# Kernel optimization log

Measured on AMD Instinct MI355X. Metric: run time of the kernel, lower is better.

## Reference

```python
import jax, jax.numpy as jnp
import numpy as np

VOCAB, EMB, MAXPOS, HID, IMG, ATT = 30522, 768, 512, 512, 2048, 256
LN_EPS = 1e-12


def bert_embed(ids, word_emb, pos_emb, type_emb, ln_g, ln_b):
    # ids: [..., L]; BERT embeddings = word + position + token_type(0), then LayerNorm
    L = ids.shape[-1]
    x = word_emb[ids] + pos_emb[:L] + type_emb[0]
    mu = jnp.mean(x, axis=-1, keepdims=True)
    var = jnp.mean((x - mu) ** 2, axis=-1, keepdims=True)
    return ln_g * (x - mu) * jax.lax.rsqrt(var + LN_EPS) + ln_b


def setup_inputs() -> dict:
    key = jax.random.key(0)
    ks = jax.random.split(key, 24)
    B, L, S, H = 32, 512, 6, 128
    u = lambda k, shape: jax.random.uniform(k, shape, jnp.float32, -0.1, 0.1)
    inp = {
        "separate_images": jax.random.normal(ks[0], (B, S, IMG), jnp.float32),
        "img_pred": jax.random.normal(ks[1], (B, IMG), jnp.float32),
        "input_text": jax.random.randint(ks[2], (B, L), 0, VOCAB),
        "prev_hist": jax.random.randint(ks[3], (B, S, H), 0, VOCAB),
        "prev_hist_len": jax.random.randint(ks[4], (B, S), 0, H),
        "masks": jnp.zeros((B, L), dtype=bool),
        # BERT embedding params
        "word_emb": jax.random.normal(ks[5], (VOCAB, EMB), jnp.float32) * 0.02,
        "pos_emb": jax.random.normal(ks[6], (MAXPOS, EMB), jnp.float32) * 0.02,
        "type_emb": jax.random.normal(ks[7], (2, EMB), jnp.float32) * 0.02,
        "ln_g": jnp.ones((EMB,), jnp.float32),
        "ln_b": jnp.zeros((EMB,), jnp.float32),
        # model linears (weights stored input-major: [in, out])
        "W_sep": u(ks[8], (IMG, HID)), "b_sep": jnp.zeros((HID,), jnp.float32),
        "W_e2h": u(ks[9], (EMB, HID)), "b_e2h": jnp.zeros((HID,), jnp.float32),
        "W_hist": u(ks[10], (EMB, HID)), "b_hist": jnp.zeros((HID,), jnp.float32),
        "W_img": u(ks[11], (IMG, HID)), "b_img": jnp.zeros((HID,), jnp.float32),
        "W_mm": u(ks[12], (2 * HID, HID)), "b_mm": jnp.zeros((HID,), jnp.float32),
        "W_a1": u(ks[13], (HID, ATT)), "b_a1": jnp.zeros((ATT,), jnp.float32),
        "W_a2": u(ks[14], (ATT, 1)), "b_a2": jnp.zeros((1,), jnp.float32),
        "W_f1": u(ks[15], (2 * HID, HID)), "b_f1": jnp.zeros((HID,), jnp.float32),
        "W_f2": u(ks[16], (HID, 2)), "b_f2": jnp.zeros((2,), jnp.float32),
    }
    return inp


def reference(separate_images, img_pred, input_text, prev_hist, prev_hist_len, masks,
              word_emb, pos_emb, type_emb, ln_g, ln_b,
              W_sep, b_sep, W_e2h, b_e2h, W_hist, b_hist, W_img, b_img,
              W_mm, b_mm, W_a1, b_a1, W_a2, b_a2, W_f1, b_f1, W_f2, b_f2):
    relu = jax.nn.relu
    # utterance path
    reps = bert_embed(input_text, word_emb, pos_emb, type_emb, ln_g, ln_b)  # [B,L,E]
    input_reps = relu(reps @ W_e2h + b_e2h)                                 # [B,L,H]
    proj_img = relu(img_pred @ W_img + b_img)                               # [B,H]
    rep_img = jnp.broadcast_to(proj_img[:, None, :], input_reps.shape)
    mm_reps = relu(jnp.concatenate([input_reps, rep_img], axis=2) @ W_mm + b_mm)
    att = jnp.tanh(mm_reps @ W_a1 + b_a1) @ W_a2 + b_a2                     # [B,L,1]
    att = jnp.where(masks[:, :, None], -jnp.inf, att)
    w = jax.nn.softmax(att, axis=1)
    attended = jnp.sum(mm_reps * w, axis=1)                                 # [B,H]
    # image / history path
    sep = separate_images @ W_sep + b_sep                                   # [B,6,H]
    H = prev_hist.shape[-1]
    hist_emb = bert_embed(prev_hist, word_emb, pos_emb, type_emb, ln_g, ln_b)  # [B,6,Hl,E]
    valid = (jnp.arange(H) < prev_hist_len[..., None]).astype(hist_emb.dtype)  # [B,6,Hl]
    denom = jnp.maximum(prev_hist_len, 1).astype(hist_emb.dtype)[..., None]
    hist_avg = jnp.einsum('bshe,bsh->bse', hist_emb, valid) / denom
    contrib = relu(hist_avg @ W_hist + b_hist) * (prev_hist_len[..., None] > 0)
    sep = relu(sep + contrib)
    sep = sep / jnp.maximum(jnp.linalg.norm(sep, axis=2, keepdims=True), 1e-12)
    sep = sep.mean(axis=1)                                                  # [B,H]
    h = jnp.concatenate([sep, attended], axis=1) @ W_f1 + b_f1
    h = jax.nn.gelu(h, approximate=False)
    return h @ W_f2 + b_f2
```

## Files before the change

kernel.cpp:

```cpp
#include <hip/hip_runtime.h>
#include <hip/hip_bf16.h>
#include <math.h>

#define VOCAB 30522
#define EMB 768
#define MAXPOS 512
#define HID 512
#define IMG 2048
#define ATT 256
#define BB 32
#define LL 512
#define SS 6
#define HL 128
#define LN_EPS 1e-12f
#define KCH 128
#define NROWS (BB * LL)
#define MPS (BB + BB * SS)

typedef __bf16 bf16_t;
typedef __attribute__((ext_vector_type(4))) __bf16 bf16x4;
typedef __attribute__((ext_vector_type(8))) __bf16 bf16x8;
typedef __attribute__((ext_vector_type(4))) float f32x4;

#define AS1 __attribute__((address_space(1)))
#define AS3 __attribute__((address_space(3)))
__device__ __forceinline__ void gload_lds16(const bf16_t* g, bf16_t* l) {
    __builtin_amdgcn_global_load_lds((const AS1 void*)g, (AS3 void*)l, 16, 0, 0);
}

__device__ __forceinline__ float wave_sum(float v) {
    v += __shfl_xor(v, 1);  v += __shfl_xor(v, 2);  v += __shfl_xor(v, 4);
    v += __shfl_xor(v, 8);  v += __shfl_xor(v, 16); v += __shfl_xor(v, 32);
    return v;
}
__device__ __forceinline__ float wave_max(float v) {
    v = fmaxf(v, __shfl_xor(v, 1));  v = fmaxf(v, __shfl_xor(v, 2));
    v = fmaxf(v, __shfl_xor(v, 4));  v = fmaxf(v, __shfl_xor(v, 8));
    v = fmaxf(v, __shfl_xor(v, 16)); v = fmaxf(v, __shfl_xor(v, 32));
    return v;
}


__device__ void dev_embed2(int r0, const int* __restrict__ ids,
                           const float* __restrict__ we, const float* __restrict__ pe,
                           const float* __restrict__ te, const float* __restrict__ g,
                           const float* __restrict__ bta, bf16_t* __restrict__ out) {
    int lane = threadIdx.x & 63;
    int r1 = r0 + 1;
    int id0 = ids[r0], id1 = ids[r1];
    const float* w0 = we + (size_t)id0 * EMB + lane * 12;
    const float* p0 = pe + (size_t)(r0 & (LL - 1)) * EMB + lane * 12;
    const float* w1 = we + (size_t)id1 * EMB + lane * 12;
    const float* p1 = pe + (size_t)(r1 & (LL - 1)) * EMB + lane * 12;
    const float* tp = te + lane * 12;
    float4 a0[3], b0[3], a1[3], b1[3], c[3];
#pragma unroll
    for (int q = 0; q < 3; q++) {
        a0[q] = *(const float4*)(w0 + q * 4);
        a1[q] = *(const float4*)(w1 + q * 4);
        b0[q] = *(const float4*)(p0 + q * 4);
        b1[q] = *(const float4*)(p1 + q * 4);
        c[q]  = *(const float4*)(tp + q * 4);
    }
    const float* gp = g + lane * 12;
    const float* bp = bta + lane * 12;
#pragma unroll
    for (int rr = 0; rr < 2; rr++) {
        float4* av = rr ? a1 : a0;
        float4* bv = rr ? b1 : b0;
        int r = rr ? r1 : r0;
        float x[12]; float s = 0.f, ss = 0.f;
#pragma unroll
        for (int q = 0; q < 3; q++) {
            float v0 = av[q].x + bv[q].x + c[q].x;
            float v1 = av[q].y + bv[q].y + c[q].y;
            float v2 = av[q].z + bv[q].z + c[q].z;
            float v3 = av[q].w + bv[q].w + c[q].w;
            x[q * 4 + 0] = v0; x[q * 4 + 1] = v1;
            x[q * 4 + 2] = v2; x[q * 4 + 3] = v3;
            s += v0 + v1 + v2 + v3;
            ss += v0 * v0 + v1 * v1 + v2 * v2 + v3 * v3;
        }
        s = wave_sum(s); ss = wave_sum(ss);
        float mu = s * (1.0f / EMB);
        float var = ss * (1.0f / EMB) - mu * mu;
        float rs = rsqrtf(var + LN_EPS);
        bf16_t* orow = out + (size_t)r * EMB + lane * 12;
#pragma unroll
        for (int q = 0; q < 3; q++) {
            float4 gv = *(const float4*)(gp + q * 4);
            float4 bb = *(const float4*)(bp + q * 4);
            bf16x4 y;
            y[0] = (bf16_t)(gv.x * (x[q * 4 + 0] - mu) * rs + bb.x);
            y[1] = (bf16_t)(gv.y * (x[q * 4 + 1] - mu) * rs + bb.y);
            y[2] = (bf16_t)(gv.z * (x[q * 4 + 2] - mu) * rs + bb.z);
            y[3] = (bf16_t)(gv.w * (x[q * 4 + 3] - mu) * rs + bb.w);
            *(bf16x4*)(orow + q * 4) = y;
        }
    }
}

__device__ void dev_conv(const float* __restrict__ in, bf16_t* __restrict__ out,
                         int K, int N, int x, int y, char* smem) {
    float (*t)[33] = (float(*)[33])smem;
    int n0 = x * 32, k0 = y * 32;
    int tx = threadIdx.x & 31, ty = threadIdx.x >> 5;
#pragma unroll
    for (int i = 0; i < 4; i++)
        t[ty + i * 8][tx] = in[(size_t)(k0 + ty + i * 8) * N + n0 + tx];
    __syncthreads();
#pragma unroll
    for (int i = 0; i < 4; i++)
        out[(size_t)(n0 + ty + i * 8) * K + k0 + tx] = (bf16_t)t[tx][ty + i * 8];
}

__device__ void dev_hist(int bs, int grp, const int* __restrict__ ids,
                         const int* __restrict__ lens,
                         const float* __restrict__ we, const float* __restrict__ pe,
                         const float* __restrict__ te, const float* __restrict__ g,
                         const float* __restrict__ bta,
                         float* __restrict__ parts, char* smem) {
    float (*acc)[EMB] = (float(*)[EMB])smem;
    int len = lens[bs];
    int tid = threadIdx.x, wid = tid >> 6, lane = tid & 63;
#pragma unroll
    for (int k = 0; k < 12; k++) acc[wid][lane + k * 64] = 0.f;
#pragma unroll
    for (int i = 0; i < 4; i++) {
        int h = grp + 8 * wid + 32 * i;
        if (h >= len) continue;
        int id = ids[bs * HL + h];
        const float* wrow = we + (size_t)id * EMB;
        const float* prow = pe + (size_t)h * EMB;
        float x[12]; float s = 0.f, ss = 0.f;
#pragma unroll
        for (int k = 0; k < 12; k++) {
            int j = lane + k * 64;
            float v = wrow[j] + prow[j] + te[j];
            x[k] = v; s += v; ss += v * v;
        }
        s = wave_sum(s); ss = wave_sum(ss);
        float mu = s * (1.0f / EMB);
        float var = ss * (1.0f / EMB) - mu * mu;
        float rs = rsqrtf(var + LN_EPS);
#pragma unroll
        for (int k = 0; k < 12; k++) {
            int j = lane + k * 64;
            acc[wid][j] += g[j] * (x[k] - mu) * rs + bta[j];
        }
    }
    __syncthreads();
    float* dst = parts + ((size_t)grp * (BB * SS) + bs) * EMB;
    for (int j = tid; j < EMB; j += 256)
        dst[j] = acc[0][j] + acc[1][j] + acc[2][j] + acc[3][j];
}

template <int AMODE>
__device__ void dev_thin(int bx, int by, int bz,
                         const float* __restrict__ A, int lda,
                         const float* __restrict__ parts, size_t MNp,
                         const float* __restrict__ abias,
                         const int* __restrict__ lens,
                         const float* __restrict__ B, int ldb,
                         float* __restrict__ part, int M, int N, char* smem) {
    float (*As)[KCH] = (float(*)[KCH])smem;
    int tid = threadIdx.x;
    int n0 = bx * 256, m0 = by * 16, k0 = bz * KCH;

    if (AMODE == 0) {
#pragma unroll
        for (int i = 0; i < 2; i++) {
            int lin = (i * 256 + tid) * 4;
            int m = lin >> 7, k = lin & (KCH - 1);
            *(float4*)&As[m][k] = *(const float4*)(A + (size_t)(m0 + m) * lda + k0 + k);
        }
    } else if (AMODE == 1) {
#pragma unroll
        for (int i = 0; i < 2; i++) {
            int f = i * 256 + tid;
            int m = f >> 5, kq = (f & 31) * 4;
            int row = m0 + m;
            float4 v = *(const float4*)(abias + k0 + kq);
#pragma unroll
            for (int ks = 0; ks < 16; ks++) {
                float4 p = *(const float4*)(parts + (size_t)ks * MNp +
                                            (size_t)row * 512 + k0 + kq);
                v.x += p.x; v.y += p.y; v.z += p.z; v.w += p.w;
            }
            v.x = fmaxf(v.x, 0.f); v.y = fmaxf(v.y, 0.f);
            v.z = fmaxf(v.z, 0.f); v.w = fmaxf(v.w, 0.f);
            *(float4*)&As[m][kq] = v;
        }
    } else {
#pragma unroll
        for (int i = 0; i < 2; i++) {
            int f = i * 256 + tid;
            int m = f >> 5, kq = (f & 31) * 4;
            int row = m0 + m;
            float invd = 1.0f / fmaxf((float)lens[row], 1.0f);
            float4 v = {};
#pragma unroll
            for (int gg = 0; gg < 8; gg++) {
                float4 p = *(const float4*)(parts + (size_t)gg * MNp +
                                            (size_t)row * EMB + k0 + kq);
                v.x += p.x; v.y += p.y; v.z += p.z; v.w += p.w;
            }
            As[m][kq + 0] = v.x * invd; As[m][kq + 1] = v.y * invd;
            As[m][kq + 2] = v.z * invd; As[m][kq + 3] = v.w * invd;
        }
    }
    __syncthreads();
    int nq = tid & 63, mg = tid >> 6;
    const float* Bp = B + (size_t)k0 * ldb + n0 + nq * 4;
    float4 acc[4] = {};
    for (int kk = 0; kk < KCH; kk += 8) {
        float4 b0 = *(const float4*)(Bp + (size_t)(kk + 0) * ldb);
        float4 b1 = *(const float4*)(Bp + (size_t)(kk + 1) * ldb);
        float4 b2 = *(const float4*)(Bp + (size_t)(kk + 2) * ldb);
        float4 b3 = *(const float4*)(Bp + (size_t)(kk + 3) * ldb);
        float4 b4 = *(const float4*)(Bp + (size_t)(kk + 4) * ldb);
        float4 b5 = *(const float4*)(Bp + (size_t)(kk + 5) * ldb);
        float4 b6 = *(const float4*)(Bp + (size_t)(kk + 6) * ldb);
        float4 b7 = *(const float4*)(Bp + (size_t)(kk + 7) * ldb);
        float4 bv[8] = {b0, b1, b2, b3, b4, b5, b6, b7};
#pragma unroll
        for (int j = 0; j < 8; j++) {
#pragma unroll
            for (int mi = 0; mi < 4; mi++) {
                float a = As[mg * 4 + mi][kk + j];
                acc[mi].x += a * bv[j].x; acc[mi].y += a * bv[j].y;
                acc[mi].z += a * bv[j].z; acc[mi].w += a * bv[j].w;
            }
        }
    }
    size_t MN = (size_t)M * N;
#pragma unroll
    for (int mi = 0; mi < 4; mi++)
        *(float4*)(part + (size_t)bz * MN +
                   (size_t)(m0 + mg * 4 + mi) * N + n0 + nq * 4) = acc[mi];
}

template <int ACT, bool OBF16, bool ROWADD4, bool FUSE_ATT>
__device__ void dev_mfma(int bx, int by,
                         const bf16_t* __restrict__ A, const bf16_t* __restrict__ Bt,
                         const float* __restrict__ bias,
                         const float* __restrict__ rowadd,
                         void* __restrict__ Cv,
                         const float* __restrict__ w2, float* __restrict__ att_part,
                         int M, int N, int K, char* smem) {
    bf16_t* As = (bf16_t*)smem;
    bf16_t* Bs = (bf16_t*)(smem + 16384);
    float (*attp)[2] = (float(*)[2])(smem + 32768);
    int tid = threadIdx.x;
    int lane = tid & 63, wid = tid >> 6;
    int wr = wid >> 1, wc = wid & 1;
    int row0 = by * 128, col0 = bx * 128;

    int srow = tid >> 2;
    int sslot = tid & 3;

    const bf16_t* Ag = A + (size_t)row0 * K;
    const bf16_t* Bg = Bt + (size_t)col0 * K;

    f32x4 acc[4][4] = {};
    int lrow = lane & 15;
    int g8 = lane >> 4;

    auto stage_pair = [&](int buf, int kb) {
#pragma unroll
        for (int rr = 0; rr < 2; rr++) {
            int r = srow + rr * 64;
            int sl = sslot ^ ((r >> 1) & 3);
            gload_lds16(Ag + (size_t)r * K + kb + sl * 8,
                        As + buf * 4096 + wid * 512 + rr * 2048);
            gload_lds16(Bg + (size_t)r * K + kb + sl * 8,
                        Bs + buf * 4096 + wid * 512 + rr * 2048);
        }
    };

    stage_pair(0, 0);
    __syncthreads();
    int cur = 0;
    for (int kb = 0; kb < K; kb += 32) {
        if (kb + 32 < K) stage_pair(cur ^ 1, kb + 32);
        bf16x8 af[4], bfr[4];
#pragma unroll
        for (int mi = 0; mi < 4; mi++) {
            int r = wr * 64 + mi * 16 + lrow;
            int sl = g8 ^ ((r >> 1) & 3);
            af[mi] = *(const bf16x8*)(As + cur * 4096 + r * 32 + sl * 8);
        }
#pragma unroll
        for (int ni = 0; ni < 4; ni++) {
            int r = wc * 64 + ni * 16 + lrow;
            int sl = g8 ^ ((r >> 1) & 3);
            bfr[ni] = *(const bf16x8*)(Bs + cur * 4096 + r * 32 + sl * 8);
        }
#pragma unroll
        for (int mi = 0; mi < 4; mi++)
#pragma unroll
            for (int ni = 0; ni < 4; ni++)
                acc[mi][ni] = __builtin_amdgcn_mfma_f32_16x16x32_bf16(
                    af[mi], bfr[ni], acc[mi][ni], 0, 0, 0);
        __syncthreads();
        cur ^= 1;
    }

    if (FUSE_ATT) {
        float w2v[4];
#pragma unroll
        for (int ni = 0; ni < 4; ni++)
            w2v[ni] = w2[col0 + wc * 64 + ni * 16 + lrow];
#pragma unroll
        for (int mi = 0; mi < 4; mi++) {
#pragma unroll
            for (int r = 0; r < 4; r++) {
                float s = 0.f;
#pragma unroll
                for (int ni = 0; ni < 4; ni++) {
                    int col = col0 + wc * 64 + ni * 16 + lrow;
                    float v = tanhf(acc[mi][ni][r] + bias[col]);
                    s += v * w2v[ni];
                }
                s += __shfl_xor(s, 1); s += __shfl_xor(s, 2);
                s += __shfl_xor(s, 4); s += __shfl_xor(s, 8);
                if ((lane & 15) == 0)
                    attp[wr * 64 + mi * 16 + (lane >> 4) * 4 + r][wc] = s;
            }
        }
        __syncthreads();
        if (tid < 128)
            att_part[(size_t)bx * M + row0 + tid] = attp[tid][0] + attp[tid][1];
        return;
    }

    float* Cf = (float*)Cv;
    bf16_t* Cb = (bf16_t*)Cv;
    int rg = (lane >> 4) * 4;
#pragma unroll
    for (int mi = 0; mi < 4; mi++) {
#pragma unroll
        for (int ni = 0; ni < 4; ni++) {
            int col = col0 + wc * 64 + ni * 16 + lrow;
#pragma unroll
            for (int r = 0; r < 4; r++) {
                int row = row0 + wr * 64 + mi * 16 + rg + r;
                float v = acc[mi][ni][r] + bias[col];
                if (ROWADD4) {
                    int bslot = row >> 9;
#pragma unroll
                    for (int ks = 0; ks < 4; ks++)
                        v += rowadd[(size_t)ks * BB * HID + (size_t)bslot * HID + col];
                }
                if (ACT == 1) v = fmaxf(v, 0.f);
                if (ACT == 2) v = tanhf(v);
                if (OBF16) Cb[(size_t)row * N + col] = (bf16_t)v;
                else       Cf[(size_t)row * N + col] = v;
            }
        }
    }
}


#define D1_EMB   2048
#define D1_HIST  (D1_EMB + 1536)
#define D1_CONV  (D1_HIST + 768)
#define D1_T4A   (D1_CONV + 64)
#define D1_T4B   (D1_T4A + 384)
__global__ __launch_bounds__(256)
void uber_pre(const int* input_text, const int* prev_hist, const int* prev_hist_ln,
              const float* word_emb, const float* pos_emb, const float* type_emb,
              const float* ln_g, const float* ln_b,
              const float* W_e2h, bf16_t* Wt_e2h,
              const float* W_mm, bf16_t* Wt_mm,
              const float* W_a1, bf16_t* Wt_a1,
              const float* img_pred, const float* sep_images,
              const float* W_img, const float* W_sep,
              bf16_t* reps_bf, float* hist_parts, float* partA) {
    __shared__ __align__(16) char smem[12288];
    int bid = blockIdx.x;
    if (bid < D1_EMB) {
        int r0 = (bid * 4 + (threadIdx.x >> 6)) * 2;
        dev_embed2(r0, input_text, word_emb, pos_emb, type_emb, ln_g, ln_b, reps_bf);
    } else if (bid < D1_HIST) {
        int b = bid - D1_EMB;
        dev_hist(b >> 3, b & 7, prev_hist, prev_hist_ln, word_emb, pos_emb,
                 type_emb, ln_g, ln_b, hist_parts, smem);
    } else if (bid < D1_CONV) {
        int b = bid - D1_HIST;
        if (b < 384)      dev_conv(W_e2h, Wt_e2h, EMB, HID, b & 15, b >> 4, smem);
        else if (b < 640) { int c = b - 384; dev_conv(W_mm, Wt_mm, HID, HID, c & 15, c >> 4, smem); }
        else              { int c = b - 640; dev_conv(W_a1, Wt_a1, HID, ATT, c & 7, c >> 3, smem); }
    } else if (bid < D1_T4A) {
        int l = bid - D1_CONV;
        dev_thin<0>(l & 1, (l >> 1) & 1, l >> 2, img_pred, IMG,
                    nullptr, 0, nullptr, nullptr, W_img, HID, partA, MPS, HID, smem);
    } else {
        int l = bid - D1_T4A;
        int l2 = l >> 1;
        dev_thin<0>(l & 1, l2 % 12, l2 / 12, sep_images, IMG,
                    nullptr, 0, nullptr, nullptr, W_sep, HID,
                    partA + (size_t)BB * HID, MPS, HID, smem);
    }
}

#define D2_MF   512
#define D2_IMG2 (D2_MF + 16)
#define D2_HG   (D2_IMG2 + 144)
__global__ __launch_bounds__(256)
void uber_gemm1(const bf16_t* reps_bf, const bf16_t* Wt_e2h, const float* b_e2h,
                bf16_t* input_reps,
                const float* partA, const float* b_img, const float* W_mm,
                float* partC,
                const float* hist_parts, const int* prev_hist_ln,
                const float* W_hist, float* partB) {
    __shared__ __align__(16) char smem[33792];
    int bid = blockIdx.x;
    if (bid < D2_MF) {
        dev_mfma<1, true, false, false>(bid & 3, bid >> 2, reps_bf, Wt_e2h, b_e2h,
                                        nullptr, input_reps, nullptr, nullptr,
                                        NROWS, HID, EMB, smem);
    } else if (bid < D2_IMG2) {
        int l = bid - D2_MF;
        dev_thin<1>(l & 1, (l >> 1) & 1, l >> 2, nullptr, 0,
                    partA, (size_t)MPS * HID, b_img, nullptr,
                    W_mm + (size_t)HID * HID, HID, partC, BB, HID, smem);
    } else {
        int l = bid - D2_IMG2;
        int l2 = l >> 1;
        dev_thin<2>(l & 1, l2 % 12, l2 / 12, nullptr, 0,
                    hist_parts, (size_t)BB * SS * EMB, nullptr, prev_hist_ln,
                    W_hist, HID, partB, BB * SS, HID, smem);
    }
}

__global__ __launch_bounds__(256)
void mfma_mm_k(const bf16_t* input_reps, const bf16_t* Wt_mm, const float* b_mm,
               const float* partC, bf16_t* mm_reps) {
    __shared__ __align__(16) char smem[33792];
    dev_mfma<1, true, true, false>(blockIdx.x & 3, blockIdx.x >> 2, input_reps,
                                   Wt_mm, b_mm, partC, mm_reps, nullptr, nullptr,
                                   NROWS, HID, HID, smem);
}

__global__ __launch_bounds__(256)
void mfma_a1_k(const bf16_t* mm_reps, const bf16_t* Wt_a1, const float* b_a1,
               const float* W_a2, float* att_part) {
    __shared__ __align__(16) char smem[33792];
    dev_mfma<2, false, false, true>(blockIdx.x & 1, blockIdx.x >> 1, mm_reps,
                                    Wt_a1, b_a1, nullptr, nullptr, W_a2, att_part,
                                    NROWS, ATT, HID, smem);
}

__global__ void attend_sep(const float* __restrict__ att_part,
                           const unsigned char* __restrict__ masks,
                           const float* __restrict__ b2,
                           const bf16_t* __restrict__ mm,
                           const float* __restrict__ pA,
                           const float* __restrict__ pB,
                           const float* __restrict__ b_sep,
                           const float* __restrict__ b_hist,
                           const int* __restrict__ lens,
                           float* __restrict__ xcat) {
    int bid = blockIdx.x;
    int tid = threadIdx.x, wid = tid >> 6, lane = tid & 63;
    __shared__ float wsm[LL];
    __shared__ float arr[4];
    __shared__ float red[4][64];
    if (bid < 256) {
        int b = bid >> 3, hc = bid & 7;
        int l0 = tid, l1 = tid + 256;
        float v0 = att_part[b * LL + l0] + att_part[(size_t)NROWS + b * LL + l0] + b2[0];
        float v1 = att_part[b * LL + l1] + att_part[(size_t)NROWS + b * LL + l1] + b2[0];
        if (masks[b * LL + l0]) v0 = -INFINITY;
        if (masks[b * LL + l1]) v1 = -INFINITY;
        float m = wave_max(fmaxf(v0, v1));
        if (lane == 0) arr[wid] = m;
        __syncthreads();
        float M = fmaxf(fmaxf(arr[0], arr[1]), fmaxf(arr[2], arr[3]));
        float e0 = expf(v0 - M), e1 = expf(v1 - M);
        wsm[l0] = e0; wsm[l1] = e1;
        float s = wave_sum(e0 + e1);
        __syncthreads();
        if (lane == 0) arr[wid] = s;
        __syncthreads();
        float inv = 1.0f / (arr[0] + arr[1] + arr[2] + arr[3]);
        int h = hc * 64 + lane;
        const bf16_t* base = mm + (size_t)b * LL * HID + h;
        float acc = 0.f;
        int ls = wid * 128;
#pragma unroll 4
        for (int l = ls; l < ls + 128; l++)
            acc += (float)base[(size_t)l * HID] * wsm[l];
        red[wid][lane] = acc;
        __syncthreads();
        if (wid == 0)
            xcat[b * 1024 + 512 + h] =
                (red[0][lane] + red[1][lane] + red[2][lane] + red[3][lane]) * inv;
    } else {
        int b = bid - 256;
        const size_t MNa = (size_t)MPS * HID;
        const size_t MNb = (size_t)BB * SS * HID;
        float acc0 = 0.f, acc1 = 0.f;
        for (int s = 0; s < SS; s++) {
            int idx = b * SS + s;
            int len = lens[idx];
            size_t baseA = (size_t)(BB + idx) * HID;
            size_t baseB = (size_t)idx * HID;
            float v0 = b_sep[tid], v1 = b_sep[tid + 256];
#pragma unroll
            for (int ks = 0; ks < 16; ks++) {
                v0 += pA[ks * MNa + baseA + tid];
                v1 += pA[ks * MNa + baseA + tid + 256];
            }
            float c0 = b_hist[tid], c1 = b_hist[tid + 256];
#pragma unroll
            for (int ks = 0; ks < 6; ks++) {
                c0 += pB[ks * MNb + baseB + tid];
                c1 += pB[ks * MNb + baseB + tid + 256];
            }
            c0 = fmaxf(c0, 0.f); c1 = fmaxf(c1, 0.f);
            if (len <= 0) { c0 = 0.f; c1 = 0.f; }
            float y0 = fmaxf(v0 + c0, 0.f), y1 = fmaxf(v1 + c1, 0.f);
            float ssq = wave_sum(y0 * y0 + y1 * y1);
            if (lane == 0) arr[wid] = ssq;
            __syncthreads();
            float tot = arr[0] + arr[1] + arr[2] + arr[3];
            float inv = 1.0f / fmaxf(sqrtf(tot), 1e-12f);
            acc0 += y0 * inv; acc1 += y1 * inv;
            __syncthreads();
        }
        xcat[b * 1024 + tid] = acc0 * (1.0f / SS);
        xcat[b * 1024 + 256 + tid] = acc1 * (1.0f / SS);
    }
}

__global__ __launch_bounds__(256)
void thin_f1_k(const float* xcat, const float* W_f1, float* partD) {
    __shared__ __align__(16) char smem[8192];
    int l = blockIdx.x;
    dev_thin<0>(l & 1, (l >> 1) & 1, l >> 2, xcat, 1024,
                nullptr, 0, nullptr, nullptr, W_f1, HID, partD, BB, HID, smem);
}

__global__ void final_out2(const float* __restrict__ part,
                           const float* __restrict__ b1,
                           const float* __restrict__ W2,
                           const float* __restrict__ b2,
                           float* __restrict__ out) {
    int b = blockIdx.x;
    int tid = threadIdx.x;
    __shared__ float h[HID];
    const size_t MN = (size_t)BB * HID;
#pragma unroll
    for (int jj = 0; jj < 2; jj++) {
        int d = tid + jj * 256;
        float a = b1[d];
#pragma unroll
        for (int ks = 0; ks < 8; ks++) a += part[ks * MN + (size_t)b * HID + d];
        h[d] = 0.5f * a * (1.0f + erff(a * 0.70710678118654752f));
    }
    __syncthreads();
    float p0 = 0.f, p1 = 0.f;
    for (int j = tid; j < HID; j += 256) {
        float hv = h[j];
        p0 += hv * W2[j * 2 + 0];
        p1 += hv * W2[j * 2 + 1];
    }
    p0 = wave_sum(p0); p1 = wave_sum(p1);
    __shared__ float r0[4], r1[4];
    int wid = tid >> 6;
    if ((tid & 63) == 0) { r0[wid] = p0; r1[wid] = p1; }
    __syncthreads();
    if (tid == 0) {
        out[b * 2 + 0] = r0[0] + r0[1] + r0[2] + r0[3] + b2[0];
        out[b * 2 + 1] = r1[0] + r1[1] + r1[2] + r1[3] + b2[1];
    }
}

extern "C" void kernel_launch(void* const* d_in, const int* in_sizes, int n_in,
                              void* d_out, int out_size, void* d_ws, size_t ws_size,
                              hipStream_t stream) {
    const float* sep_images   = (const float*)d_in[0];
    const float* img_pred     = (const float*)d_in[1];
    const int*   input_text   = (const int*)d_in[2];
    const int*   prev_hist    = (const int*)d_in[3];
    const int*   prev_hist_ln = (const int*)d_in[4];
    const unsigned char* masks = (const unsigned char*)d_in[5];
    const float* word_emb = (const float*)d_in[6];
    const float* pos_emb  = (const float*)d_in[7];
    const float* type_emb = (const float*)d_in[8];
    const float* ln_g = (const float*)d_in[9];
    const float* ln_b = (const float*)d_in[10];
    const float* W_sep = (const float*)d_in[11]; const float* b_sep = (const float*)d_in[12];
    const float* W_e2h = (const float*)d_in[13]; const float* b_e2h = (const float*)d_in[14];
    const float* W_hist = (const float*)d_in[15]; const float* b_hist = (const float*)d_in[16];
    const float* W_img = (const float*)d_in[17]; const float* b_img = (const float*)d_in[18];
    const float* W_mm = (const float*)d_in[19]; const float* b_mm = (const float*)d_in[20];
    const float* W_a1 = (const float*)d_in[21]; const float* b_a1 = (const float*)d_in[22];
    const float* W_a2 = (const float*)d_in[23]; const float* b_a2 = (const float*)d_in[24];
    const float* W_f1 = (const float*)d_in[25]; const float* b_f1 = (const float*)d_in[26];
    const float* W_f2 = (const float*)d_in[27]; const float* b_f2 = (const float*)d_in[28];

    char* ws = (char*)d_ws;
    size_t o = 0;
    auto alloc = [&](size_t bytes) { void* p = ws + o; o += (bytes + 255) & ~(size_t)255; return p; };

    bf16_t* reps_bf     = (bf16_t*)alloc((size_t)NROWS * EMB * 2);
    bf16_t* input_reps  = (bf16_t*)alloc((size_t)NROWS * HID * 2);
    bf16_t* mm_reps     = (bf16_t*)alloc((size_t)NROWS * HID * 2);
    float*  att_part    = (float*)alloc((size_t)2 * NROWS * 4);
    float*  xcat        = (float*)alloc((size_t)BB * 1024 * 4);
    float*  hist_parts  = (float*)alloc((size_t)8 * BB * SS * EMB * 4);
    bf16_t* Wt_e2h      = (bf16_t*)alloc((size_t)EMB * HID * 2);
    bf16_t* Wt_mm       = (bf16_t*)alloc((size_t)HID * HID * 2);
    bf16_t* Wt_a1       = (bf16_t*)alloc((size_t)HID * ATT * 2);
    float*  partA       = (float*)alloc((size_t)16 * MPS * HID * 4);
    float*  partB       = (float*)alloc((size_t)6 * BB * SS * HID * 4);
    float*  partC       = (float*)alloc((size_t)4 * BB * HID * 4);
    float*  partD       = (float*)alloc((size_t)8 * BB * HID * 4);

    uber_pre<<<D1_T4B, 256, 0, stream>>>(
        input_text, prev_hist, prev_hist_ln, word_emb, pos_emb, type_emb,
        ln_g, ln_b, W_e2h, Wt_e2h, W_mm, Wt_mm, W_a1, Wt_a1,
        img_pred, sep_images, W_img, W_sep, reps_bf, hist_parts, partA);

    uber_gemm1<<<D2_HG, 256, 0, stream>>>(
        reps_bf, Wt_e2h, b_e2h, input_reps,
        partA, b_img, W_mm, partC,
        hist_parts, prev_hist_ln, W_hist, partB);

    mfma_mm_k<<<512, 256, 0, stream>>>(input_reps, Wt_mm, b_mm, partC, mm_reps);

    mfma_a1_k<<<256, 256, 0, stream>>>(mm_reps, Wt_a1, b_a1, W_a2, att_part);

    attend_sep<<<288, 256, 0, stream>>>(att_part, masks, b_a2, mm_reps,
                                        partA, partB, b_sep, b_hist,
                                        prev_hist_ln, xcat);

    thin_f1_k<<<32, 256, 0, stream>>>(xcat, W_f1, partD);

    final_out2<<<BB, 256, 0, stream>>>(partD, b_f1, W_f2, b_f2, (float*)d_out);
}
```

Baseline: 144.5 us.

## Rebalance fused kernel stages to overlap history work with GEMMs

Moves the history-embedding LayerNorm and the separate-image thin GEMM out of the first fused kernel into the e2h GEMM kernel. Moves the history-projection thin GEMM into the mm GEMM kernel, which drops one separate launch. The aim is to balance per-stage work so memory-bound blocks run beside compute-bound MFMA blocks, and to lower the first kernel's shared memory. This adds more heterogeneous blocks to each launch, which can cause tail imbalance or contention for LDS and occupancy.

```diff
diff --git a/kernel.cpp b/kernel.cpp
--- a/kernel.cpp
+++ b/kernel.cpp
@@ -362,85 +362,92 @@
 }
 
 
-#define D1_EMB   2048
-#define D1_HIST  (D1_EMB + 1536)
-#define D1_CONV  (D1_HIST + 768)
-#define D1_T4A   (D1_CONV + 64)
-#define D1_T4B   (D1_T4A + 384)
+#define E1_EMB   2048
+#define E1_CONV  (E1_EMB + 768)
+#define E1_TIMG  (E1_CONV + 64)
 __global__ __launch_bounds__(256)
-void uber_pre(const int* input_text, const int* prev_hist, const int* prev_hist_ln,
+void uber_pre(const int* input_text,
               const float* word_emb, const float* pos_emb, const float* type_emb,
               const float* ln_g, const float* ln_b,
               const float* W_e2h, bf16_t* Wt_e2h,
               const float* W_mm, bf16_t* Wt_mm,
               const float* W_a1, bf16_t* Wt_a1,
-              const float* img_pred, const float* sep_images,
-              const float* W_img, const float* W_sep,
-              bf16_t* reps_bf, float* hist_parts, float* partA) {
-    __shared__ __align__(16) char smem[12288];
+              const float* img_pred, const float* W_img,
+              bf16_t* reps_bf, float* partA) {
+    __shared__ __align__(16) char smem[8192];
     int bid = blockIdx.x;
-    if (bid < D1_EMB) {
+    if (bid < E1_EMB) {
         int r0 = (bid * 4 + (threadIdx.x >> 6)) * 2;
         dev_embed2(r0, input_text, word_emb, pos_emb, type_emb, ln_g, ln_b, reps_bf);
-    } else if (bid < D1_HIST) {
-        int b = bid - D1_EMB;
-        dev_hist(b >> 3, b & 7, prev_hist, prev_hist_ln, word_emb, pos_emb,
-                 type_emb, ln_g, ln_b, hist_parts, smem);
-    } else if (bid < D1_CONV) {
-        int b = bid - D1_HIST;
+    } else if (bid < E1_CONV) {
+        int b = bid - E1_EMB;
         if (b < 384)      dev_conv(W_e2h, Wt_e2h, EMB, HID, b & 15, b >> 4, smem);
         else if (b < 640) { int c = b - 384; dev_conv(W_mm, Wt_mm, HID, HID, c & 15, c >> 4, smem); }
         else              { int c = b - 640; dev_conv(W_a1, Wt_a1, HID, ATT, c & 7, c >> 3, smem); }
-    } else if (bid < D1_T4A) {
-        int l = bid - D1_CONV;
+    } else {
+        int l = bid - E1_CONV;
         dev_thin<0>(l & 1, (l >> 1) & 1, l >> 2, img_pred, IMG,
                     nullptr, 0, nullptr, nullptr, W_img, HID, partA, MPS, HID, smem);
-    } else {
-        int l = bid - D1_T4A;
+    }
+}
+
+#define E2_MF   512
+#define E2_HIST (E2_MF + 1536)
+#define E2_SEP  (E2_HIST + 384)
+#define E2_IMG2 (E2_SEP + 16)
+__global__ __launch_bounds__(256)
+void uber_gemm1(const bf16_t* reps_bf, const bf16_t* Wt_e2h, const float* b_e2h,
+                bf16_t* input_reps,
+                const int* prev_hist, const int* prev_hist_ln,
+                const float* word_emb, const float* pos_emb, const float* type_emb,
+                const float* ln_g, const float* ln_b, float* hist_parts,
+                const float* sep_images, const float* W_sep,
+                float* partA, const float* b_img, const float* W_mm,
+                float* partC) {
+    __shared__ __align__(16) char smem[33792];
+    int bid = blockIdx.x;
+    if (bid < E2_MF) {
+        dev_mfma<1, true, false, false>(bid & 3, bid >> 2, reps_bf, Wt_e2h, b_e2h,
+                                        nullptr, input_reps, nullptr, nullptr,
+                                        NROWS, HID, EMB, smem);
+    } else if (bid < E2_HIST) {
+        int b = bid - E2_MF;
+        dev_hist(b >> 3, b & 7, prev_hist, prev_hist_ln, word_emb, pos_emb,
+                 type_emb, ln_g, ln_b, hist_parts, smem);
+    } else if (bid < E2_SEP) {
+        int l = bid - E2_HIST;
         int l2 = l >> 1;
         dev_thin<0>(l & 1, l2 % 12, l2 / 12, sep_images, IMG,
                     nullptr, 0, nullptr, nullptr, W_sep, HID,
                     partA + (size_t)BB * HID, MPS, HID, smem);
-    }
-}
-
-#define D2_MF   512
-#define D2_IMG2 (D2_MF + 16)
-#define D2_HG   (D2_IMG2 + 144)
+    } else {
+        int l = bid - E2_SEP;
+        dev_thin<1>(l & 1, (l >> 1) & 1, l >> 2, nullptr, 0,
+                    partA, (size_t)MPS * HID, b_img, nullptr,
+                    W_mm + (size_t)HID * HID, HID, partC, BB, HID, smem);
+    }
+}
+
+#define E3_MF 512
+#define E3_HG (E3_MF + 144)
 __global__ __launch_bounds__(256)
-void uber_gemm1(const bf16_t* reps_bf, const bf16_t* Wt_e2h, const float* b_e2h,
-                bf16_t* input_reps,
-                const float* partA, const float* b_img, const float* W_mm,
-                float* partC,
+void uber_gemm2(const bf16_t* input_reps, const bf16_t* Wt_mm, const float* b_mm,
+                const float* partC, bf16_t* mm_reps,
                 const float* hist_parts, const int* prev_hist_ln,
                 const float* W_hist, float* partB) {
     __shared__ __align__(16) char smem[33792];
     int bid = blockIdx.x;
-    if (bid < D2_MF) {
-        dev_mfma<1, true, false, false>(bid & 3, bid >> 2, reps_bf, Wt_e2h, b_e2h,
-                                        nullptr, input_reps, nullptr, nullptr,
-                                        NROWS, HID, EMB, smem);
-    } else if (bid < D2_IMG2) {
-        int l = bid - D2_MF;
-        dev_thin<1>(l & 1, (l >> 1) & 1, l >> 2, nullptr, 0,
-                    partA, (size_t)MPS * HID, b_img, nullptr,
-                    W_mm + (size_t)HID * HID, HID, partC, BB, HID, smem);
+    if (bid < E3_MF) {
+        dev_mfma<1, true, true, false>(bid & 3, bid >> 2, input_reps,
+                                       Wt_mm, b_mm, partC, mm_reps, nullptr, nullptr,
+                                       NROWS, HID, HID, smem);
     } else {
-        int l = bid - D2_IMG2;
+        int l = bid - E3_MF;
         int l2 = l >> 1;
         dev_thin<2>(l & 1, l2 % 12, l2 / 12, nullptr, 0,
                     hist_parts, (size_t)BB * SS * EMB, nullptr, prev_hist_ln,
                     W_hist, HID, partB, BB * SS, HID, smem);
     }
-}
-
-__global__ __launch_bounds__(256)
-void mfma_mm_k(const bf16_t* input_reps, const bf16_t* Wt_mm, const float* b_mm,
-               const float* partC, bf16_t* mm_reps) {
-    __shared__ __align__(16) char smem[33792];
-    dev_mfma<1, true, true, false>(blockIdx.x & 3, blockIdx.x >> 2, input_reps,
-                                   Wt_mm, b_mm, partC, mm_reps, nullptr, nullptr,
-                                   NROWS, HID, HID, smem);
 }
 
 __global__ __launch_bounds__(256)
@@ -620,17 +627,19 @@
     float*  partC       = (float*)alloc((size_t)4 * BB * HID * 4);
     float*  partD       = (float*)alloc((size_t)8 * BB * HID * 4);
 
-    uber_pre<<<D1_T4B, 256, 0, stream>>>(
-        input_text, prev_hist, prev_hist_ln, word_emb, pos_emb, type_emb,
-        ln_g, ln_b, W_e2h, Wt_e2h, W_mm, Wt_mm, W_a1, Wt_a1,
-        img_pred, sep_images, W_img, W_sep, reps_bf, hist_parts, partA);
-
-    uber_gemm1<<<D2_HG, 256, 0, stream>>>(
+    uber_pre<<<E1_TIMG, 256, 0, stream>>>(
+        input_text, word_emb, pos_emb, type_emb, ln_g, ln_b,
+        W_e2h, Wt_e2h, W_mm, Wt_mm, W_a1, Wt_a1,
+        img_pred, W_img, reps_bf, partA);
+
+    uber_gemm1<<<E2_IMG2, 256, 0, stream>>>(
         reps_bf, Wt_e2h, b_e2h, input_reps,
-        partA, b_img, W_mm, partC,
+        prev_hist, prev_hist_ln, word_emb, pos_emb, type_emb, ln_g, ln_b,
+        hist_parts, sep_images, W_sep, partA, b_img, W_mm, partC);
+
+    uber_gemm2<<<E3_HG, 256, 0, stream>>>(
+        input_reps, Wt_mm, b_mm, partC, mm_reps,
         hist_parts, prev_hist_ln, W_hist, partB);
-
-    mfma_mm_k<<<512, 256, 0, stream>>>(input_reps, Wt_mm, b_mm, partC, mm_reps);
 
     mfma_a1_k<<<256, 256, 0, stream>>>(mm_reps, Wt_a1, b_a1, W_a2, att_part);
 
```

New measurement: 153.5 us. 1.06x slower.
